# Performance work log

Hardware: AMD Instinct MI355X
Metric: run time of the kernel (lower is better)

Reference implementation:

```python
import jax, jax.numpy as jnp
import numpy as np

B, S, D, H = 4, 2048, 512, 8
INNER = D  # assumed AttentionHead.inner_size == size (naive single-head attention)


def setup_inputs() -> dict:
    key = jax.random.key(0)
    ks = jax.random.split(key, 8)
    scale = 0.02
    return {
        "emb_input": jax.random.normal(ks[0], (B, S, D), dtype=jnp.float32),
        "Wq": jax.random.normal(ks[1], (H, D, INNER), dtype=jnp.float32) * scale,
        "bq": jnp.zeros((H, INNER), dtype=jnp.float32),
        "Wk": jax.random.normal(ks[2], (H, D, INNER), dtype=jnp.float32) * scale,
        "bk": jnp.zeros((H, INNER), dtype=jnp.float32),
        "Wv": jax.random.normal(ks[3], (H, D, INNER), dtype=jnp.float32) * scale,
        "bv": jnp.zeros((H, INNER), dtype=jnp.float32),
        "Wp": jax.random.normal(ks[4], (H * INNER, D), dtype=jnp.float32) * scale,
        "bp": jnp.zeros((D,), dtype=jnp.float32),
    }


def reference(emb_input, Wq, bq, Wk, bk, Wv, bv, Wp, bp):
    # All heads batched into one einsum instead of a Python loop over submodules.
    x = emb_input  # [B, S, D]
    q = jnp.einsum("bsd,hde->bhse", x, Wq) + bq[None, :, None, :]  # [B,H,S,E]
    k = jnp.einsum("bsd,hde->bhse", x, Wk) + bk[None, :, None, :]
    v = jnp.einsum("bsd,hde->bhse", x, Wv) + bv[None, :, None, :]
    scores = jnp.einsum("bhse,bhte->bhst", q, k) / jnp.sqrt(
        jnp.asarray(INNER, dtype=x.dtype)
    )  # [B,H,S,S]
    attn = jax.nn.softmax(scores, axis=-1)
    o = jnp.einsum("bhst,bhte->bhse", attn, v)  # [B,H,S,E]
    # concat over heads (dim=2 in torch => feature dim after per-head outputs)
    o = jnp.transpose(o, (0, 2, 1, 3)).reshape(B, S, H * INNER)
    return o @ Wp + bp  # [B, S, D]
```

## Files before the change

kernel.cpp:

```cpp
#include <hip/hip_runtime.h>


typedef short s8v __attribute__((ext_vector_type(8)));
typedef float f4v __attribute__((ext_vector_type(4)));
typedef unsigned short us;
typedef us us4v __attribute__((ext_vector_type(4)));

__device__ inline us f2b(float f) {
  union { float f; unsigned u; } v; v.f = f;
  unsigned r = v.u + 0x7FFFu + ((v.u >> 16) & 1u);
  return (us)(r >> 16);
}

__device__ inline void gld16(const us* g, us* l) {
  __builtin_amdgcn_global_load_lds(
      (const __attribute__((address_space(1))) void*)g,
      (__attribute__((address_space(3))) void*)l, 16, 0, 0);
}

__global__ __launch_bounds__(512, 2) void attn_fused(
    const us* __restrict__ Q, const us* __restrict__ Kh,
    const us* __restrict__ Vt, us* __restrict__ O,
    int Lh, float alpha) {
  constexpr int S = 2048, E = 512;
  constexpr int NCH = (S / 128) * 8;
  __shared__ __align__(16) us smem[50176];
  const int t = threadIdx.x, w = t >> 6, ln = t & 63;
  const int m16 = ln & 15, quad = ln >> 4;

  const int gx = gridDim.x;
  const int nblk = gx * gridDim.y;
  const int flat = blockIdx.x + gx * blockIdx.y;
  int nid = flat;
  if ((nblk & 7) == 0) nid = (flat & 7) * (nblk >> 3) + (flat >> 3);
  const int qt = nid % gx, zh = nid / gx;

  const long long zoff = (long long)zh * S * E;
  const us* Qz = Q + zoff;
  const us* Kz = Kh + zoff;
  const us* Vz = Vt + zoff;
  const int q0 = qt * 128;

  s8v Qf[16];
  {
    const us* qrow = Qz + (long long)(q0 + 16 * w + m16) * E + quad * 8;
#pragma unroll
    for (int kq = 0; kq < 16; ++kq) Qf[kq] = *(const s8v*)(qrow + kq * 32);
  }

  f4v accO[4][8];
#pragma unroll
  for (int e = 0; e < 4; ++e)
#pragma unroll
    for (int nb = 0; nb < 8; ++nb) accO[e][nb] = (f4v){0.f, 0.f, 0.f, 0.f};
  float la[4] = {0.f, 0.f, 0.f, 0.f};

#define STAGE(g_)                                                            \
  {                                                                          \
    const int tau_ = (g_) >> 3, sub_ = (g_) & 7;                             \
    us* dst_ = smem + ((g_) & 1) * 16384;                                    \
    _Pragma("unroll") for (int j = 0; j < 4; ++j) {                          \
      const int c_ = t + 512 * j;                                            \
      const int s_ = c_ >> 6, l_ = c_ & 63;                                  \
      const int nbm_ = ((s_ >> 2) * 16 + (l_ & 15));                         \
      const int kk_ = (s_ & 3) * 32 + (l_ >> 4) * 8;                         \
      const us* src_ = (sub_ < 4)                                            \
          ? Kz + (long long)(tau_ * 128 + nbm_) * E + sub_ * 128 + kk_       \
          : Vz + (long long)((sub_ - 4) * 128 + nbm_) * S + tau_ * 128 + kk_;\
      gld16(src_, dst_ + c_ * 8);                                            \
    }                                                                        \
  }

  STAGE(0);
  STAGE(1);

  for (int tau = 0; tau < S / 128; ++tau) {
    f4v accS[8];
#pragma unroll
    for (int nb = 0; nb < 8; ++nb) accS[nb] = (f4v){0.f, 0.f, 0.f, 0.f};
    s8v pa[4];
#pragma unroll
    for (int ph = 0; ph < 8; ++ph) {
      const int g = tau * 8 + ph;
      if (g + 1 < NCH) asm volatile("s_waitcnt vmcnt(4)" ::: "memory");
      else             asm volatile("s_waitcnt vmcnt(0)" ::: "memory");
      __builtin_amdgcn_s_barrier();
      const us* rb = smem + (g & 1) * 16384;
      __builtin_amdgcn_s_setprio(1);
#pragma unroll
      for (int ks = 0; ks < 4; ++ks) {
#pragma unroll
        for (int h = 0; h < 2; ++h) {
          s8v bf[4];
#pragma unroll
          for (int nb = 0; nb < 4; ++nb)
            bf[nb] = *(const s8v*)&rb[(((h * 4 + nb) * 4 + ks) * 64 + ln) * 8];
          if (ph < 4) {
#pragma unroll
            for (int nb = 0; nb < 4; ++nb)
              accS[h * 4 + nb] = __builtin_amdgcn_mfma_f32_16x16x32_bf16(
                  Qf[ph * 4 + ks], bf[nb], accS[h * 4 + nb], 0, 0, 0);
          } else {
#pragma unroll
            for (int nb = 0; nb < 4; ++nb)
              accO[ph - 4][h * 4 + nb] = __builtin_amdgcn_mfma_f32_16x16x32_bf16(
                  pa[ks], bf[nb], accO[ph - 4][h * 4 + nb], 0, 0, 0);
          }
        }
      }
      __builtin_amdgcn_s_setprio(0);
      __builtin_amdgcn_s_barrier();
      if (g + 2 < NCH) STAGE(g + 2);
      if (ph == 3) {
        us* pw = smem + 32768 + w * 2176;
#pragma unroll
        for (int nb = 0; nb < 8; ++nb)
#pragma unroll
          for (int gg = 0; gg < 4; ++gg) {
            accS[nb][gg] = __expf(fmaf(accS[nb][gg], alpha, -4.f));
            pw[(quad * 4 + gg) * 136 + nb * 16 + m16] = f2b(accS[nb][gg]);
          }
#pragma unroll
        for (int gg = 0; gg < 4; ++gg) {
          float s = 0.f;
#pragma unroll
          for (int nb = 0; nb < 8; ++nb) s += accS[nb][gg];
          s += __shfl_xor(s, 1, 64);
          s += __shfl_xor(s, 2, 64);
          s += __shfl_xor(s, 4, 64);
          s += __shfl_xor(s, 8, 64);
          la[gg] += s;
        }
        asm volatile("s_waitcnt lgkmcnt(0)" ::: "memory");
        __builtin_amdgcn_sched_barrier(0);
#pragma unroll
        for (int kp = 0; kp < 4; ++kp)
          pa[kp] = *(const s8v*)&pw[m16 * 136 + kp * 32 + quad * 8];
      }
    }
  }
#undef STAGE

  float inv[4];
#pragma unroll
  for (int gg = 0; gg < 4; ++gg) inv[gg] = 1.f / la[gg];
  const int b = zh >> Lh, hc = zh & ((1 << Lh) - 1);
  const int HCE = E << Lh;
  us* Ob = O + (long long)b * S * HCE + (long long)hc * E;
  us* stw = smem + w * 4288;
#pragma unroll
  for (int half = 0; half < 2; ++half) {
#pragma unroll
    for (int ec = 0; ec < 2; ++ec) {
      const int ecg = half * 2 + ec;
#pragma unroll
      for (int nb = 0; nb < 8; ++nb)
#pragma unroll
        for (int gg = 0; gg < 4; ++gg)
          stw[(quad * 4 + gg) * 268 + ec * 128 + nb * 16 + m16] =
              f2b(accO[ecg][nb][gg] * inv[gg]);
    }
    asm volatile("s_waitcnt lgkmcnt(0)" ::: "memory");
    __builtin_amdgcn_sched_barrier(0);
#pragma unroll
    for (int rp = 0; rp < 8; ++rp) {
      const int row = rp * 2 + (ln >> 5);
      const s8v v = *(const s8v*)&stw[row * 268 + (ln & 31) * 8];
      *(s8v*)&Ob[(long long)(q0 + 16 * w + row) * HCE + half * 256 +
                 (ln & 31) * 8] = v;
    }
    if (half == 0) {
      asm volatile("s_waitcnt lgkmcnt(0)" ::: "memory");
      __builtin_amdgcn_sched_barrier(0);
    }
  }
}

template <int EPI>
__global__ __launch_bounds__(512, 2) void gemm_nt(
    const us* __restrict__ A, int lda, long long sA0, long long sA1,
    const us* __restrict__ Bm, int ldb, long long sB0, long long sB1,
    const float* __restrict__ bias, const float* __restrict__ bias2,
    const float* __restrict__ bias3,
    void* __restrict__ Cv, void* __restrict__ C2, void* __restrict__ C3,
    int ldc, long long sC0, long long sC1,
    int K, float alpha, int L, int sbits) {
  __shared__ __align__(16) us As[2][16384];
  __shared__ __align__(16) us Bs[2][16384];
  const int t = threadIdx.x;
  const int wv = t >> 6, ln = t & 63;
  const int m16 = ln & 15, quad = ln >> 4;

  const int gx = gridDim.x, gxy = gx * gridDim.y;
  const int nblk = gxy * gridDim.z;
  const int flat = blockIdx.x + gx * blockIdx.y + gxy * blockIdx.z;
  int nid = flat;
  if ((nblk & 7) == 0) nid = (flat & 7) * (nblk >> 3) + (flat >> 3);
  const int bz = nid / gxy, rem = nid % gxy;
  const int by = rem / gx, bx = rem % gx;

  const long long row0 = (long long)by * 256;
  const long long col0 = (long long)bx * 256;
  const int zo = bz >> L, zi = bz & ((1 << L) - 1);
  const us* Az = A + zo * sA0 + zi * sA1;
  const us* Bz = Bm + zo * sB0 + zi * sB1;

  int offA[4], offB[4];
#pragma unroll
  for (int j = 0; j < 4; ++j) {
    const int c = t + 512 * j;
    const int s = c >> 6, l = c & 63;
    const int mb = s >> 1, ks = s & 1, qd = (l >> 4) & 3, mm = l & 15;
    offA[j] = (int)((row0 + mb * 16 + mm) * (long long)lda + ks * 32 + qd * 8);
    offB[j] = (int)((col0 + mb * 16 + mm) * (long long)ldb + ks * 32 + qd * 8);
  }

  f4v acc[8][4];
#pragma unroll
  for (int r = 0; r < 8; ++r)
#pragma unroll
    for (int c = 0; c < 4; ++c) acc[r][c] = (f4v){0.f, 0.f, 0.f, 0.f};

  const int nk = K >> 6;
  const int wr = wv >> 2, wc = wv & 3;

#define BARR __builtin_amdgcn_s_barrier()
#define LGKM0                                              \
  do {                                                     \
    asm volatile("s_waitcnt lgkmcnt(0)" ::: "memory");     \
    __builtin_amdgcn_sched_barrier(0);                     \
  } while (0)
#define READ_A(p_)                                                           \
  _Pragma("unroll") for (int rr = 0; rr < 2; ++rr)                           \
  _Pragma("unroll") for (int ks = 0; ks < 2; ++ks)                           \
      af[rr * 2 + ks] = *(const s8v*)&As[b]                                  \
          [(((wr * 8 + (p_) * 2 + rr) * 2 + ks) * 64 + ln) * 8];
#define MFMA_Q(p_)                                                           \
  __builtin_amdgcn_s_setprio(1);                                             \
  _Pragma("unroll") for (int ks = 0; ks < 2; ++ks)                           \
  _Pragma("unroll") for (int rr = 0; rr < 2; ++rr)                           \
  _Pragma("unroll") for (int c = 0; c < 4; ++c)                              \
      acc[(p_) * 2 + rr][c] = __builtin_amdgcn_mfma_f32_16x16x32_bf16(       \
          af[rr * 2 + ks], bfr[c * 2 + ks], acc[(p_) * 2 + rr][c], 0, 0, 0); \
  __builtin_amdgcn_s_setprio(0);

#pragma unroll
  for (int j = 0; j < 4; ++j) gld16(Az + offA[j], (us*)As[0] + (t + 512 * j) * 8);
#pragma unroll
  for (int j = 0; j < 4; ++j) gld16(Bz + offB[j], (us*)Bs[0] + (t + 512 * j) * 8);
  if (nk > 1) {
#pragma unroll
    for (int j = 0; j < 4; ++j)
      gld16(Bz + offB[j] + 64, (us*)Bs[1] + (t + 512 * j) * 8);
    gld16(Az + offA[0] + 64, (us*)As[1] + t * 8);
    gld16(Az + offA[2] + 64, (us*)As[1] + (t + 1024) * 8);
    asm volatile("s_waitcnt vmcnt(6)" ::: "memory");
  } else {
    asm volatile("s_waitcnt vmcnt(0)" ::: "memory");
  }
  BARR;

  for (int kt = 0; kt < nk; ++kt) {
    const int b = kt & 1;
    s8v bfr[8], af[4];
#pragma unroll
    for (int c = 0; c < 4; ++c)
#pragma unroll
      for (int ks = 0; ks < 2; ++ks)
        bfr[c * 2 + ks] =
            *(const s8v*)&Bs[b][(((wc * 4 + c) * 2 + ks) * 64 + ln) * 8];
    READ_A(0);
    if (kt + 1 < nk) {
      const int kof = (kt + 1) << 6;
      gld16(Az + offA[1] + kof, (us*)As[b ^ 1] + (t + 512) * 8);
      gld16(Az + offA[3] + kof, (us*)As[b ^ 1] + (t + 1536) * 8);
    }
    asm volatile("s_waitcnt lgkmcnt(8)" ::: "memory");
    BARR; LGKM0; MFMA_Q(0); BARR;
    READ_A(1);
    if (kt + 2 < nk) {
      const int kof = (kt + 2) << 6;
#pragma unroll
      for (int j = 0; j < 4; ++j)
        gld16(Bz + offB[j] + kof, (us*)Bs[b] + (t + 512 * j) * 8);
    }
    BARR; LGKM0; MFMA_Q(1); BARR;
    READ_A(2);
    if (kt + 2 < nk) {
      const int kof = (kt + 2) << 6;
      gld16(Az + offA[0] + kof, (us*)As[b] + t * 8);
      gld16(Az + offA[2] + kof, (us*)As[b] + (t + 1024) * 8);
    }
    BARR; LGKM0; MFMA_Q(2); BARR;
    READ_A(3);
    BARR; LGKM0; MFMA_Q(3);
    if (kt + 2 < nk) asm volatile("s_waitcnt vmcnt(6)" ::: "memory");
    else             asm volatile("s_waitcnt vmcnt(0)" ::: "memory");
    BARR;
  }
#undef READ_A
#undef MFMA_Q
#undef BARR
#undef LGKM0

#pragma unroll
  for (int r = 0; r < 8; ++r) {
    const int inRow = wr * 128 + r * 16 + quad * 4;
    const long long gr0 = row0 + inRow;
#pragma unroll
    for (int c = 0; c < 4; ++c) {
      const long long gc = col0 + wc * 64 + c * 16 + m16;
      if (EPI == 3) {
        const int which = (int)(gc >> sbits);
        const int gsec = (int)gc & ((1 << sbits) - 1);
        const int hc = gsec >> 9, e = (int)gc & 511;
        const long long slice =
            ((long long)zo * (1 << (sbits - 9)) + hc) * 1048576LL;
        if (which == 0) {
          us* C = (us*)Cv;
          const float bb = bias[gsec];
#pragma unroll
          for (int g = 0; g < 4; ++g)
            C[slice + (gr0 + g) * 512 + e] = f2b(acc[r][c][g] + bb);
        } else if (which == 1) {
          us* C = (us*)C2;
          const float bb = bias2[gsec];
#pragma unroll
          for (int g = 0; g < 4; ++g)
            C[slice + (gr0 + g) * 512 + e] = f2b(acc[r][c][g] + bb);
        } else {
          us* C = (us*)C3;
          const float bb = bias3[gsec];
          us4v pk;
#pragma unroll
          for (int g = 0; g < 4; ++g) pk[g] = f2b(acc[r][c][g] + bb);
          *(us4v*)&C[slice + (long long)e * 2048 + gr0] = pk;
        }
      } else {
        float* C = (float*)Cv + zo * sC0;
        float* p = C + gr0 * ldc + gc;
#pragma unroll
        for (int g = 0; g < 4; ++g)
          atomicAdd(&p[(long long)g * ldc], acc[r][c][g] * alpha);
      }
    }
  }
}

__global__ __launch_bounds__(256) void conv_bf16(const float* __restrict__ in,
                                                 us* __restrict__ out, int n4) {
  const int i = blockIdx.x * 256 + threadIdx.x;
  if (i < n4) {
    const float4 f = ((const float4*)in)[i];
    us4v o;
    o[0] = f2b(f.x); o[1] = f2b(f.y); o[2] = f2b(f.z); o[3] = f2b(f.w);
    ((us4v*)out)[i] = o;
  }
}

__global__ __launch_bounds__(256) void conv_transpose(const float* __restrict__ in,
                                                      us* __restrict__ out,
                                                      int R, int C, int Lc,
                                                      int mask, long long sChunk) {
  __shared__ float tile[32][33];
  const int tx = threadIdx.x & 31, ty = threadIdx.x >> 5;
  const int z = blockIdx.z;
  const long long zi = (long long)z * R * C;
  us* dst = out + (long long)(z >> Lc) * sChunk + (long long)(z & mask) * R * C;
  const int r0 = blockIdx.y * 32, c0 = blockIdx.x * 32;
#pragma unroll
  for (int j = 0; j < 4; ++j)
    tile[ty + 8 * j][tx] = in[zi + (long long)(r0 + ty + 8 * j) * C + c0 + tx];
  __syncthreads();
#pragma unroll
  for (int j = 0; j < 4; ++j)
    dst[(long long)(c0 + ty + 8 * j) * R + r0 + tx] = f2b(tile[tx][ty + 8 * j]);
}

__global__ __launch_bounds__(256) void init_out_kernel(float* __restrict__ out,
                                                       const float* __restrict__ bp,
                                                       int total) {
  const int i = blockIdx.x * 256 + threadIdx.x;
  if (i < total) out[i] = bp[i & 511];
}

extern "C" void kernel_launch(void* const* d_in, const int* in_sizes, int n_in,
                              void* d_out, int out_size, void* d_ws, size_t ws_size,
                              hipStream_t stream) {
  constexpr int Bb = 4, S = 2048, D = 512, H = 8, E = 512, HE = 4096;
  const float* x  = (const float*)d_in[0];
  const float* Wq = (const float*)d_in[1];
  const float* bq = (const float*)d_in[2];
  const float* Wk = (const float*)d_in[3];
  const float* bk = (const float*)d_in[4];
  const float* Wv = (const float*)d_in[5];
  const float* bv = (const float*)d_in[6];
  const float* Wp = (const float*)d_in[7];
  const float* bp = (const float*)d_in[8];
  float* out = (float*)d_out;

  const long long SE = (long long)S * E;
  const long long SD = (long long)S * D, ED = (long long)E * D;

  us* xh  = (us*)d_ws;
  us* W3  = xh + 4194304;
  us* WpT = W3 + 6291456;
  us* dyn = WpT + 2097152;

  const size_t fixedB = (size_t)(4194304 + 6291456 + 2097152) * 2;
  int HC = 8;
  while (HC > 1) {
    const size_t need = fixedB + (size_t)4 * HC * Bb * SE * 2;
    if (need <= ws_size) break;
    HC >>= 1;
  }
  const int Lh = (HC == 8) ? 3 : (HC == 4) ? 2 : (HC == 2) ? 1 : 0;
  const int BHC = Bb * HC;
  const int sbits = 9 + Lh;

  us* qh = dyn;
  us* kh = qh + (size_t)BHC * SE;
  us* vT = kh + (size_t)BHC * SE;
  us* oh = vT + (size_t)BHC * SE;

  const dim3 tb(256), tg(512);
  init_out_kernel<<<dim3((Bb * S * D + 255) / 256), tb, 0, stream>>>(
      out, bp, Bb * S * D);
  conv_bf16<<<dim3(4194304 / 4 / 256), tb, 0, stream>>>(x, xh, 4194304 / 4);
  const long long sChunk = 3LL * HC * ED;
  conv_transpose<<<dim3(16, 16, H), tb, 0, stream>>>(Wq, W3, D, E, Lh, HC - 1, sChunk);
  conv_transpose<<<dim3(16, 16, H), tb, 0, stream>>>(Wk, W3 + HC * ED, D, E, Lh, HC - 1, sChunk);
  conv_transpose<<<dim3(16, 16, H), tb, 0, stream>>>(Wv, W3 + 2 * HC * ED, D, E, Lh, HC - 1, sChunk);
  conv_transpose<<<dim3(16, 128, 1), tb, 0, stream>>>(Wp, WpT, HE, D, 0, 0, 0);

  const float aS = 0.044194173824159216f;
  const dim3 gQKV(3 * HC * E / 256, 8, Bb);
  const dim3 gAT(S / 128, BHC);
  const dim3 gOP(2, 8, BHC);

  for (int c = 0; c < H / HC; ++c) {
    const int h0 = c * HC;
    gemm_nt<3><<<gQKV, tg, 0, stream>>>(
        xh, D, SD, 0, W3 + c * sChunk, D, 0, 0,
        bq + h0 * E, bk + h0 * E, bv + h0 * E,
        qh, kh, vT, 512, 0, SE, D, 1.f, 0, sbits);
    attn_fused<<<gAT, tg, 0, stream>>>(qh, kh, vT, oh, Lh, aS);
    gemm_nt<5><<<gOP, tg, 0, stream>>>(
        oh, HC * E, (long long)S * HC * E, 512,
        WpT + (long long)h0 * E, HE, 0, 512,
        nullptr, nullptr, nullptr, out, nullptr, nullptr,
        D, SD, 0, 512, 1.f, Lh, 0);
  }
}
```

Measured before the change: 1.016 ms.

## Load K/V fragments directly from global instead of LDS double-buffered staging

Removes the cooperative global-to-LDS double-buffered staging of K and V tiles. Each wave now reads its K and V MFMA fragments straight from global memory. The KV tile shrinks from 128 to 64 columns, and the per-iteration block barriers are dropped. This cuts LDS footprint and synchronisation, but every wave now fetches the same K/V data independently, relying on L1/L2 for reuse, and global-load latency is exposed with no explicit prefetch.

```diff
diff --git a/kernel.cpp b/kernel.cpp
--- a/kernel.cpp
+++ b/kernel.cpp
@@ -23,8 +23,7 @@
     const us* __restrict__ Vt, us* __restrict__ O,
     int Lh, float alpha) {
   constexpr int S = 2048, E = 512;
-  constexpr int NCH = (S / 128) * 8;
-  __shared__ __align__(16) us smem[50176];
+  __shared__ __align__(16) us smem[34304];
   const int t = threadIdx.x, w = t >> 6, ln = t & 63;
   const int m16 = ln & 15, quad = ln >> 4;
 
@@ -37,8 +36,6 @@
 
   const long long zoff = (long long)zh * S * E;
   const us* Qz = Q + zoff;
-  const us* Kz = Kh + zoff;
-  const us* Vz = Vt + zoff;
   const int q0 = qt * 128;
 
   s8v Qf[16];
@@ -48,6 +45,9 @@
     for (int kq = 0; kq < 16; ++kq) Qf[kq] = *(const s8v*)(qrow + kq * 32);
   }
 
+  const us* Krow = Kh + zoff + (long long)m16 * E + quad * 8;
+  const us* Vrow = Vt + zoff + (long long)m16 * S + quad * 8;
+
   f4v accO[4][8];
 #pragma unroll
   for (int e = 0; e < 4; ++e)
@@ -55,91 +55,65 @@
     for (int nb = 0; nb < 8; ++nb) accO[e][nb] = (f4v){0.f, 0.f, 0.f, 0.f};
   float la[4] = {0.f, 0.f, 0.f, 0.f};
 
-#define STAGE(g_)                                                            \
-  {                                                                          \
-    const int tau_ = (g_) >> 3, sub_ = (g_) & 7;                             \
-    us* dst_ = smem + ((g_) & 1) * 16384;                                    \
-    _Pragma("unroll") for (int j = 0; j < 4; ++j) {                          \
-      const int c_ = t + 512 * j;                                            \
-      const int s_ = c_ >> 6, l_ = c_ & 63;                                  \
-      const int nbm_ = ((s_ >> 2) * 16 + (l_ & 15));                         \
-      const int kk_ = (s_ & 3) * 32 + (l_ >> 4) * 8;                         \
-      const us* src_ = (sub_ < 4)                                            \
-          ? Kz + (long long)(tau_ * 128 + nbm_) * E + sub_ * 128 + kk_       \
-          : Vz + (long long)((sub_ - 4) * 128 + nbm_) * S + tau_ * 128 + kk_;\
-      gld16(src_, dst_ + c_ * 8);                                            \
-    }                                                                        \
-  }
-
-  STAGE(0);
-  STAGE(1);
-
-  for (int tau = 0; tau < S / 128; ++tau) {
-    f4v accS[8];
-#pragma unroll
-    for (int nb = 0; nb < 8; ++nb) accS[nb] = (f4v){0.f, 0.f, 0.f, 0.f};
-    s8v pa[4];
-#pragma unroll
-    for (int ph = 0; ph < 8; ++ph) {
-      const int g = tau * 8 + ph;
-      if (g + 1 < NCH) asm volatile("s_waitcnt vmcnt(4)" ::: "memory");
-      else             asm volatile("s_waitcnt vmcnt(0)" ::: "memory");
-      __builtin_amdgcn_s_barrier();
-      const us* rb = smem + (g & 1) * 16384;
-      __builtin_amdgcn_s_setprio(1);
-#pragma unroll
-      for (int ks = 0; ks < 4; ++ks) {
-#pragma unroll
-        for (int h = 0; h < 2; ++h) {
-          s8v bf[4];
-#pragma unroll
-          for (int nb = 0; nb < 4; ++nb)
-            bf[nb] = *(const s8v*)&rb[(((h * 4 + nb) * 4 + ks) * 64 + ln) * 8];
-          if (ph < 4) {
-#pragma unroll
-            for (int nb = 0; nb < 4; ++nb)
-              accS[h * 4 + nb] = __builtin_amdgcn_mfma_f32_16x16x32_bf16(
-                  Qf[ph * 4 + ks], bf[nb], accS[h * 4 + nb], 0, 0, 0);
-          } else {
-#pragma unroll
-            for (int nb = 0; nb < 4; ++nb)
-              accO[ph - 4][h * 4 + nb] = __builtin_amdgcn_mfma_f32_16x16x32_bf16(
-                  pa[ks], bf[nb], accO[ph - 4][h * 4 + nb], 0, 0, 0);
-          }
-        }
+  us* pw = smem + w * 1088;
+
+  for (int tau = 0; tau < S / 64; ++tau) {
+    const int kv0 = tau * 64;
+    f4v accS[4];
+#pragma unroll
+    for (int nb = 0; nb < 4; ++nb) accS[nb] = (f4v){0.f, 0.f, 0.f, 0.f};
+#pragma unroll
+    for (int ks = 0; ks < 16; ++ks) {
+      s8v kf[4];
+#pragma unroll
+      for (int nb = 0; nb < 4; ++nb)
+        kf[nb] = *(const s8v*)(Krow + (long long)(kv0 + nb * 16) * E + ks * 32);
+#pragma unroll
+      for (int nb = 0; nb < 4; ++nb)
+        accS[nb] = __builtin_amdgcn_mfma_f32_16x16x32_bf16(
+            Qf[ks], kf[nb], accS[nb], 0, 0, 0);
+    }
+#pragma unroll
+    for (int nb = 0; nb < 4; ++nb)
+#pragma unroll
+      for (int gg = 0; gg < 4; ++gg) {
+        accS[nb][gg] = __expf(fmaf(accS[nb][gg], alpha, -4.f));
+        pw[(quad * 4 + gg) * 68 + nb * 16 + m16] = f2b(accS[nb][gg]);
       }
-      __builtin_amdgcn_s_setprio(0);
-      __builtin_amdgcn_s_barrier();
-      if (g + 2 < NCH) STAGE(g + 2);
-      if (ph == 3) {
-        us* pw = smem + 32768 + w * 2176;
-#pragma unroll
-        for (int nb = 0; nb < 8; ++nb)
-#pragma unroll
-          for (int gg = 0; gg < 4; ++gg) {
-            accS[nb][gg] = __expf(fmaf(accS[nb][gg], alpha, -4.f));
-            pw[(quad * 4 + gg) * 136 + nb * 16 + m16] = f2b(accS[nb][gg]);
-          }
-#pragma unroll
-        for (int gg = 0; gg < 4; ++gg) {
-          float s = 0.f;
-#pragma unroll
-          for (int nb = 0; nb < 8; ++nb) s += accS[nb][gg];
-          s += __shfl_xor(s, 1, 64);
-          s += __shfl_xor(s, 2, 64);
-          s += __shfl_xor(s, 4, 64);
-          s += __shfl_xor(s, 8, 64);
-          la[gg] += s;
-        }
-        asm volatile("s_waitcnt lgkmcnt(0)" ::: "memory");
-        __builtin_amdgcn_sched_barrier(0);
-#pragma unroll
-        for (int kp = 0; kp < 4; ++kp)
-          pa[kp] = *(const s8v*)&pw[m16 * 136 + kp * 32 + quad * 8];
+#pragma unroll
+    for (int gg = 0; gg < 4; ++gg) {
+      float s = accS[0][gg] + accS[1][gg] + accS[2][gg] + accS[3][gg];
+      s += __shfl_xor(s, 1, 64);
+      s += __shfl_xor(s, 2, 64);
+      s += __shfl_xor(s, 4, 64);
+      s += __shfl_xor(s, 8, 64);
+      la[gg] += s;
+    }
+    asm volatile("s_waitcnt lgkmcnt(0)" ::: "memory");
+    __builtin_amdgcn_sched_barrier(0);
+    s8v pa0 = *(const s8v*)&pw[m16 * 68 + quad * 8];
+    s8v pa1 = *(const s8v*)&pw[m16 * 68 + 32 + quad * 8];
+#pragma unroll
+    for (int cb4 = 0; cb4 < 8; ++cb4) {
+      s8v vf[8];
+#pragma unroll
+      for (int j = 0; j < 4; ++j) {
+        const int cb = cb4 * 4 + j;
+        vf[j * 2]     = *(const s8v*)(Vrow + (long long)(cb * 16) * S + kv0);
+        vf[j * 2 + 1] = *(const s8v*)(Vrow + (long long)(cb * 16) * S + kv0 + 32);
       }
-    }
-  }
-#undef STAGE
+#pragma unroll
+      for (int j = 0; j < 4; ++j) {
+        const int cb = cb4 * 4 + j;
+        accO[cb >> 3][cb & 7] = __builtin_amdgcn_mfma_f32_16x16x32_bf16(
+            pa0, vf[j * 2], accO[cb >> 3][cb & 7], 0, 0, 0);
+        accO[cb >> 3][cb & 7] = __builtin_amdgcn_mfma_f32_16x16x32_bf16(
+            pa1, vf[j * 2 + 1], accO[cb >> 3][cb & 7], 0, 0, 0);
+      }
+    }
+  }
+
+  __syncthreads();
 
   float inv[4];
 #pragma unroll
```

After: 2.249 ms. 121% more time.
